# Optimization experiments

Hardware: AMD Instinct MI355X
Metric: run time of the kernel (lower is better)

The kernel has to match this reference:

```python
import jax, jax.numpy as jnp
import numpy as np

N_EDGE_TYPES = 25
EF = 2  # edge feature dim (excluding type)
HID = 10


def _edge_nn(et, ef, emb, wh, bh, wg, bg):
    # y = relu(emb[et] * (ef@Wh+bh) + (ef@Wg+bg)) -> [E, in*out]
    return jax.nn.relu(emb[et] * (ef @ wh + bh) + (ef @ wg + bg))


def _nnconv(x, et, ef, src, dst, emb, wh, bh, wg, bg, root, bias, in_c, out_c):
    n = x.shape[0]
    w = _edge_nn(et, ef, emb, wh, bh, wg, bg).reshape(-1, in_c, out_c)  # [E,in,out]
    msg = jnp.einsum('ei,eio->eo', x[src], w)                          # per-edge matmul
    s = jax.ops.segment_sum(msg, dst, num_segments=n)
    cnt = jax.ops.segment_sum(jnp.ones((src.shape[0],), x.dtype), dst, num_segments=n)
    agg = s / jnp.maximum(cnt, 1.0)[:, None]                           # scatter-mean
    return agg + x @ root + bias


def _make_params(key, in_c, out_c):
    ks = jax.random.split(key, 6)
    d = in_c * out_c
    s = 0.1
    return dict(
        emb=jax.random.normal(ks[0], (N_EDGE_TYPES, d), jnp.float32) * s,
        wh=jax.random.normal(ks[1], (EF, d), jnp.float32) * s,
        bh=jax.random.normal(ks[2], (d,), jnp.float32) * s,
        wg=jax.random.normal(ks[3], (EF, d), jnp.float32) * s,
        bg=jax.random.normal(ks[4], (d,), jnp.float32) * s,
        root=jax.random.normal(ks[5], (in_c, out_c), jnp.float32) * s,
        bias=jnp.zeros((out_c,), jnp.float32),
    )


def setup_inputs() -> dict:
    key = jax.random.key(0)
    ks = jax.random.split(key, 12)
    N, E, IN_C, OUT_C, B = 50000, 250000, 16, 16, 8
    inp = {
        'x': jax.random.normal(ks[0], (N, IN_C), jnp.float32),
        'edge_feat': jax.random.normal(ks[1], (E, EF), jnp.float32),
        'edge_type': jax.random.randint(ks[2], (E,), 0, N_EDGE_TYPES),
        'edge_src': jax.random.randint(ks[3], (E,), 0, N),
        'edge_dst': jax.random.randint(ks[4], (E,), 0, N),
        'cell_type': jax.random.randint(ks[5], (N,), 0, 3),
        'batch_ids': jnp.sort(jax.random.randint(ks[6], (N,), 0, B)),
        'batch_size': B,
    }
    for i, (ic, oc) in enumerate([(IN_C, HID), (HID, HID), (HID, OUT_C)], start=1):
        p = _make_params(ks[6 + i], ic, oc)
        for k, v in p.items():
            inp[f'{k}{i}'] = v
    return inp


def reference(x, edge_feat,
              emb1, wh1, bh1, wg1, bg1, root1, bias1,
              emb2, wh2, bh2, wg2, bg2, root2, bias2,
              emb3, wh3, bh3, wg3, bg3, root3, bias3,
              edge_type, edge_src, edge_dst, cell_type, batch_ids, batch_size):
    in_c, out_c = x.shape[1], root3.shape[1]
    h = _nnconv(x, edge_type, edge_feat, edge_src, edge_dst,
                emb1, wh1, bh1, wg1, bg1, root1, bias1, in_c, HID)
    h = jax.nn.relu(h)  # dropout is identity in eval mode
    h = _nnconv(h, edge_type, edge_feat, edge_src, edge_dst,
                emb2, wh2, bh2, wg2, bg2, root2, bias2, HID, HID)
    h = jax.nn.relu(h)
    h = _nnconv(h, edge_type, edge_feat, edge_src, edge_dst,
                emb3, wh3, bh3, wg3, bg3, root3, bias3, HID, out_c)
    h = jax.nn.relu(h)
    # scatter-mean pooling over nodes with cell_type==1, grouped by graph id
    gate = (cell_type == 1).astype(jnp.int32)
    idx = gate * (batch_ids.astype(jnp.int32) + 1)  # 0 = discarded bucket
    nseg = batch_size + 1
    s = jax.ops.segment_sum(h, idx, num_segments=nseg)
    cnt = jax.ops.segment_sum(jnp.ones((h.shape[0],), h.dtype), idx, num_segments=nseg)
    pooled = s / jnp.maximum(cnt, 1.0)[:, None]
    return pooled[1:batch_size + 1, :]  # [B, out_c]
```

## Files before the change

### kernel.cpp

```cpp
#include <hip/hip_runtime.h>

#define IN1 16
#define HIDC 10
#define OUT3 16
#define NTYPES 25
#define MAXB 32
#define HSTR 12

__global__ __launch_bounds__(256) void zero2_kernel(int* __restrict__ a, int na,
                                                    int* __restrict__ b, int nb) {
  int i = blockIdx.x * blockDim.x + threadIdx.x;
  int s = gridDim.x * blockDim.x;
  for (int j = i; j < na; j += s) a[j] = 0;
  for (int j = i; j < nb; j += s) b[j] = 0;
}

__global__ __launch_bounds__(256) void hist_kernel(const int* __restrict__ edst,
                                                   int* __restrict__ deg,
                                                   int* __restrict__ pos, int E) {
  int e = blockIdx.x * blockDim.x + threadIdx.x;
  if (e < E) pos[e] = atomicAdd(&deg[edst[e]], 1);
}

__global__ __launch_bounds__(1024) void scan_kernel(const int4* __restrict__ deg4,
                                                    int* __restrict__ row_ptr, int N) {
  __shared__ int wsums[16];
  __shared__ int s_run;
  int tid = threadIdx.x, lane = tid & 63, wid = tid >> 6;
  if (tid == 0) s_run = 0;
  __syncthreads();
  int N4 = (N + 3) >> 2;
  for (int base = 0; base < N4; base += 1024) {
    int i4 = base + tid;
    int4 v = make_int4(0, 0, 0, 0);
    if (i4 < N4) v = deg4[i4];
    int idx0 = i4 * 4;
    if (idx0 + 1 >= N) v.y = 0;
    if (idx0 + 2 >= N) v.z = 0;
    if (idx0 + 3 >= N) v.w = 0;
    int s = v.x + v.y + v.z + v.w;
    int x = s;
    #pragma unroll
    for (int off = 1; off < 64; off <<= 1) {
      int y = __shfl_up(x, off);
      if (lane >= off) x += y;
    }
    if (lane == 63) wsums[wid] = x;
    __syncthreads();
    if (tid < 16) {
      int w = wsums[tid];
      #pragma unroll
      for (int off = 1; off < 16; off <<= 1) {
        int y = __shfl_up(w, off);
        if (tid >= off) w += y;
      }
      wsums[tid] = w;
    }
    __syncthreads();
    int excl = x - s + ((wid > 0) ? wsums[wid - 1] : 0) + s_run;
    int total = wsums[15];
    if (idx0 < N) row_ptr[idx0] = excl;
    if (idx0 + 1 < N) row_ptr[idx0 + 1] = excl + v.x;
    if (idx0 + 2 < N) row_ptr[idx0 + 2] = excl + v.x + v.y;
    if (idx0 + 3 < N) row_ptr[idx0 + 3] = excl + v.x + v.y + v.z;
    __syncthreads();
    if (tid == 0) s_run += total;
    __syncthreads();
  }
  if (threadIdx.x == 0) row_ptr[N] = s_run;
}

__global__ __launch_bounds__(256) void permute_kernel(
    const int* __restrict__ edst, const int* __restrict__ esrc,
    const int* __restrict__ et, const float2* __restrict__ ef,
    const int* __restrict__ row_ptr, const int* __restrict__ pos,
    int4* __restrict__ edges, int E) {
  int e = blockIdx.x * blockDim.x + threadIdx.x;
  if (e >= E) return;
  int d = edst[e];
  int idx = row_ptr[d] + pos[e];
  float2 f = ef[e];
  int4 r;
  r.x = esrc[e];
  r.y = et[e];
  r.z = __float_as_int(f.x);
  r.w = __float_as_int(f.y);
  edges[idx] = r;
}

template<int IN_C, int XSTR, int O>
__device__ void pack_one(int t, const float* emb, const float* wh, const float* bh,
                         const float* wg, const float* bg,
                         float4* gAB, float2* gC) {
  constexpr int D = IN_C * O;
  constexpr int NI2 = XSTR / 2;
  for (int idx = threadIdx.x; idx < NI2 * O; idx += 256) {
    int i2 = idx / O, o = idx - i2 * O;
    int i0 = 2 * i2, i1 = 2 * i2 + 1;
    float a0 = 0.f, b0 = 0.f, c0 = 0.f, a1 = 0.f, b1 = 0.f, c1 = 0.f;
    if (i0 < IN_C) {
      int k = i0 * O + o;
      float e = emb[t * D + k];
      a0 = fmaf(e, wh[k], wg[k]);
      b0 = fmaf(e, wh[D + k], wg[D + k]);
      c0 = fmaf(e, bh[k], bg[k]);
    }
    if (i1 < IN_C) {
      int k = i1 * O + o;
      float e = emb[t * D + k];
      a1 = fmaf(e, wh[k], wg[k]);
      b1 = fmaf(e, wh[D + k], wg[D + k]);
      c1 = fmaf(e, bh[k], bg[k]);
    }
    int kk = (i2 * NTYPES + t) * O + o;
    gAB[kk] = make_float4(a0, b0, a1, b1);
    gC[kk] = make_float2(c0, c1);
  }
}

__global__ __launch_bounds__(256) void abc_pack_kernel(
    const float* __restrict__ emb1, const float* __restrict__ wh1,
    const float* __restrict__ bh1, const float* __restrict__ wg1, const float* __restrict__ bg1,
    const float* __restrict__ emb2, const float* __restrict__ wh2,
    const float* __restrict__ bh2, const float* __restrict__ wg2, const float* __restrict__ bg2,
    const float* __restrict__ emb3, const float* __restrict__ wh3,
    const float* __restrict__ bh3, const float* __restrict__ wg3, const float* __restrict__ bg3,
    float4* __restrict__ gAB1, float2* __restrict__ gC1,
    float4* __restrict__ gAB2, float2* __restrict__ gC2,
    float4* __restrict__ gAB3, float2* __restrict__ gC3)
{
  int t = blockIdx.x;
  pack_one<IN1, 16, HIDC>(t, emb1, wh1, bh1, wg1, bg1, gAB1, gC1);
  pack_one<HIDC, HSTR, HIDC>(t, emb2, wh2, bh2, wg2, bg2, gAB2, gC2);
  pack_one<HIDC, HSTR, OUT3>(t, emb3, wh3, bh3, wg3, bg3, gAB3, gC3);
}

template<int IN_C, int XSTR, int O, int IPG, int NPW, bool POOL>
__global__ __launch_bounds__(512, 6) void layer_kernel(
    const float* __restrict__ xin,
    const int4* __restrict__ edges,
    const int* __restrict__ row_ptr,
    const float4* __restrict__ gAB,
    const float2* __restrict__ gC,
    const float* __restrict__ root,
    const float* __restrict__ bias,
    float* __restrict__ hout,
    const int* __restrict__ ctype, const int* __restrict__ bids,
    float* __restrict__ pcnt, int N, int B)
{
  constexpr int NI2 = XSTR / 2;
  constexpr int SZ = NI2 * NTYPES * O;
  constexpr int IC = XSTR / IPG;
  constexpr int NPB = 8 * NPW;
  __shared__ __align__(16) float4 s_AB[SZ];
  __shared__ __align__(16) float2 s_C[SZ];
  __shared__ float s_root[IN_C * O];
  __shared__ float s_bias[O];
  __shared__ float s_psum[POOL ? (MAXB * 16) : 1];
  __shared__ float s_pcnt[POOL ? MAXB : 1];

  int tid = threadIdx.x;
  for (int k = tid; k < SZ; k += 512) s_AB[k] = gAB[k];
  {
    const float4* gc4 = (const float4*)gC;
    float4* sc4 = (float4*)s_C;
    for (int k = tid; k < SZ / 2; k += 512) sc4[k] = gc4[k];
  }
  for (int k = tid; k < IN_C * O; k += 512) s_root[k] = root[k];
  if (tid < O) s_bias[tid] = bias[tid];
  if (POOL) {
    for (int i = tid; i < MAXB * 16; i += 512) s_psum[i] = 0.f;
    for (int i = tid; i < MAXB; i += 512) s_pcnt[i] = 0.f;
  }
  __syncthreads();

  int wave = tid >> 6, lane = tid & 63;
  int slot = lane / (16 * IPG);
  int rem = lane % (16 * IPG);
  int ig = rem >> 4;
  int o = rem & 15;
  int oc = (o < O) ? o : (O - 1);

  int n = blockIdx.x * NPB + wave * NPW + slot;
  int start = 0, end = 0;
  if (n < N) { start = row_ptr[n]; end = row_ptr[n + 1]; }
  float acc = 0.f;
  int4 r = (start < end) ? edges[start] : make_int4(0, 0, 0, 0);
  for (int e = start; e < end;) {
    int4 cur = r;
    ++e;
    if (e < end) r = edges[e];
    int src = cur.x, t = cur.y;
    float f0 = __int_as_float(cur.z), f1 = __int_as_float(cur.w);
    const float* __restrict__ xr = xin + (size_t)src * XSTR + ig * IC;
    float xv[IC];
    if (IC == 4) {
      float4 v = *(const float4*)xr;
      xv[0] = v.x; xv[1] = v.y; xv[2] = v.z; xv[3] = v.w;
    } else {
      const float2* x2 = (const float2*)xr;
      float2 a = x2[0], b = x2[1], c = x2[2];
      xv[0] = a.x; xv[1] = a.y; xv[2] = b.x; xv[3] = b.y; xv[4] = c.x; xv[5] = c.y;
    }
    #pragma unroll
    for (int j = 0; j < IC / 2; ++j) {
      int i2 = ig * (IC / 2) + j;
      int k = (i2 * NTYPES + t) * O + oc;
      float4 ab = s_AB[k];
      float2 c2 = s_C[k];
      float w0 = fmaxf(fmaf(f0, ab.x, fmaf(f1, ab.y, c2.x)), 0.f);
      float w1 = fmaxf(fmaf(f0, ab.z, fmaf(f1, ab.w, c2.y)), 0.f);
      acc = fmaf(xv[2 * j], w0, acc);
      acc = fmaf(xv[2 * j + 1], w1, acc);
    }
  }
  acc += __shfl_xor(acc, 16);
  if (IPG == 4) acc += __shfl_xor(acc, 32);

  if (n < N && ig == 0 && o < O) {
    float inv = 1.0f / fmaxf((float)(end - start), 1.0f);
    float v = fmaf(acc, inv, s_bias[o]);
    const float* __restrict__ xr = xin + (size_t)n * XSTR;
    #pragma unroll
    for (int i = 0; i < IN_C; ++i) v = fmaf(xr[i], s_root[i * O + o], v);
    v = fmaxf(v, 0.f);
    if (!POOL) {
      hout[(size_t)n * HSTR + o] = v;
    } else if (ctype[n] == 1) {
      int b = bids[n];
      atomicAdd(&s_psum[b * 16 + o], v);
      if (o == 0) atomicAdd(&s_pcnt[b], 1.0f);
    }
  }

  if (POOL) {
    __syncthreads();
    for (int i = tid; i < B * 16; i += 512) {
      float v = s_psum[i];
      if (v != 0.f) atomicAdd(&hout[i], v);
    }
    for (int i = tid; i < B; i += 512) {
      float c = s_pcnt[i];
      if (c != 0.f) atomicAdd(&pcnt[i], c);
    }
  }
}

__global__ __launch_bounds__(256) void finalize_kernel(
    const float* __restrict__ psum, const float* __restrict__ pcnt,
    float* __restrict__ out, int B) {
  int i = blockIdx.x * blockDim.x + threadIdx.x;
  if (i >= B * OUT3) return;
  int b = i / OUT3;
  out[i] = psum[i] / fmaxf(pcnt[b], 1.0f);
}

extern "C" void kernel_launch(void* const* d_in, const int* in_sizes, int n_in,
                              void* d_out, int out_size, void* d_ws, size_t ws_size,
                              hipStream_t stream)
{
  const float* x     = (const float*)d_in[0];
  const float* ef    = (const float*)d_in[1];
  const int*   et    = (const int*)d_in[2];
  const int*   esrc  = (const int*)d_in[3];
  const int*   edst  = (const int*)d_in[4];
  const int*   ctype = (const int*)d_in[5];
  const int*   bids  = (const int*)d_in[6];
  const float* emb1 = (const float*)d_in[8];
  const float* wh1  = (const float*)d_in[9];
  const float* bh1  = (const float*)d_in[10];
  const float* wg1  = (const float*)d_in[11];
  const float* bg1  = (const float*)d_in[12];
  const float* root1= (const float*)d_in[13];
  const float* bias1= (const float*)d_in[14];
  const float* emb2 = (const float*)d_in[15];
  const float* wh2  = (const float*)d_in[16];
  const float* bh2  = (const float*)d_in[17];
  const float* wg2  = (const float*)d_in[18];
  const float* bg2  = (const float*)d_in[19];
  const float* root2= (const float*)d_in[20];
  const float* bias2= (const float*)d_in[21];
  const float* emb3 = (const float*)d_in[22];
  const float* wh3  = (const float*)d_in[23];
  const float* bh3  = (const float*)d_in[24];
  const float* wg3  = (const float*)d_in[25];
  const float* bg3  = (const float*)d_in[26];
  const float* root3= (const float*)d_in[27];
  const float* bias3= (const float*)d_in[28];

  const int N = in_sizes[0] / IN1;
  const int E = in_sizes[2];
  const int B = out_size / OUT3;

  int4* edges   = (int4*)d_ws;
  int*  deg     = (int*)(edges + E);
  int*  pos     = deg + N;
  int*  row_ptr = pos + E;
  int   np1r    = ((N + 1 + 3) / 4) * 4;
  float* h1     = (float*)(row_ptr + np1r);
  float* h2     = h1 + (size_t)N * HSTR;
  float* psum   = h2 + (size_t)N * HSTR;
  float* pcnt   = psum + (size_t)B * 16;
  float* pk     = pcnt + B;
  float4* gAB1 = (float4*)pk;
  float2* gC1  = (float2*)(pk + 8000);
  float4* gAB2 = (float4*)(pk + 12000);
  float2* gC2  = (float2*)(pk + 18000);
  float4* gAB3 = (float4*)(pk + 21000);
  float2* gC3  = (float2*)(pk + 30600);

  zero2_kernel<<<128, 256, 0, stream>>>(deg, N, (int*)psum, B * 16 + B);
  abc_pack_kernel<<<NTYPES, 256, 0, stream>>>(
      emb1, wh1, bh1, wg1, bg1, emb2, wh2, bh2, wg2, bg2, emb3, wh3, bh3, wg3, bg3,
      gAB1, gC1, gAB2, gC2, gAB3, gC3);
  hist_kernel<<<(E + 255) / 256, 256, 0, stream>>>(edst, deg, pos, E);
  scan_kernel<<<1, 1024, 0, stream>>>((const int4*)deg, row_ptr, N);
  permute_kernel<<<(E + 255) / 256, 256, 0, stream>>>(
      edst, esrc, et, (const float2*)ef, row_ptr, pos, edges, E);

  layer_kernel<IN1, 16, HIDC, 4, 1, false><<<(N + 7) / 8, 512, 0, stream>>>(
      x, edges, row_ptr, gAB1, gC1, root1, bias1, h1, nullptr, nullptr, nullptr, N, B);
  layer_kernel<HIDC, HSTR, HIDC, 2, 2, false><<<(N + 15) / 16, 512, 0, stream>>>(
      h1, edges, row_ptr, gAB2, gC2, root2, bias2, h2, nullptr, nullptr, nullptr, N, B);
  layer_kernel<HIDC, HSTR, OUT3, 2, 2, true><<<(N + 15) / 16, 512, 0, stream>>>(
      h2, edges, row_ptr, gAB3, gC3, root3, bias3, psum, ctype, bids, pcnt, N, B);

  finalize_kernel<<<1, 256, 0, stream>>>(psum, pcnt, (float*)d_out, B);
}
```

Baseline: 301.4 us.

## Fuse zeroing into pack kernel, trim padded pairs, unroll edge loop by two

Merges the zeroing kernel into the parameter-pack kernel, saving one launch. The packed tables now cover only the real input channels instead of the padded stride, which shrinks shared memory and removes wasted FMAs for layers 2 and 3. The edge loop is unrolled by two with independent accumulators to raise memory-level parallelism, replacing the explicit one-ahead prefetch. The IPG=2 split becomes uneven (3 pairs versus 2), which adds lane imbalance and a predicated branch.

```diff
diff --git a/kernel.cpp b/kernel.cpp
--- a/kernel.cpp
+++ b/kernel.cpp
@@ -6,14 +6,6 @@
 #define NTYPES 25
 #define MAXB 32
 #define HSTR 12
-
-__global__ __launch_bounds__(256) void zero2_kernel(int* __restrict__ a, int na,
-                                                    int* __restrict__ b, int nb) {
-  int i = blockIdx.x * blockDim.x + threadIdx.x;
-  int s = gridDim.x * blockDim.x;
-  for (int j = i; j < na; j += s) a[j] = 0;
-  for (int j = i; j < nb; j += s) b[j] = 0;
-}
 
 __global__ __launch_bounds__(256) void hist_kernel(const int* __restrict__ edst,
                                                    int* __restrict__ deg,
@@ -88,37 +80,29 @@
   edges[idx] = r;
 }
 
-template<int IN_C, int XSTR, int O>
+template<int IN_C, int O>
 __device__ void pack_one(int t, const float* emb, const float* wh, const float* bh,
                          const float* wg, const float* bg,
                          float4* gAB, float2* gC) {
   constexpr int D = IN_C * O;
-  constexpr int NI2 = XSTR / 2;
+  constexpr int NI2 = IN_C / 2;
   for (int idx = threadIdx.x; idx < NI2 * O; idx += 256) {
     int i2 = idx / O, o = idx - i2 * O;
-    int i0 = 2 * i2, i1 = 2 * i2 + 1;
-    float a0 = 0.f, b0 = 0.f, c0 = 0.f, a1 = 0.f, b1 = 0.f, c1 = 0.f;
-    if (i0 < IN_C) {
-      int k = i0 * O + o;
-      float e = emb[t * D + k];
-      a0 = fmaf(e, wh[k], wg[k]);
-      b0 = fmaf(e, wh[D + k], wg[D + k]);
-      c0 = fmaf(e, bh[k], bg[k]);
-    }
-    if (i1 < IN_C) {
-      int k = i1 * O + o;
-      float e = emb[t * D + k];
-      a1 = fmaf(e, wh[k], wg[k]);
-      b1 = fmaf(e, wh[D + k], wg[D + k]);
-      c1 = fmaf(e, bh[k], bg[k]);
-    }
+    int k0 = (2 * i2) * O + o, k1 = k0 + O;
+    float e0 = emb[t * D + k0], e1 = emb[t * D + k1];
+    float a0 = fmaf(e0, wh[k0], wg[k0]);
+    float b0 = fmaf(e0, wh[D + k0], wg[D + k0]);
+    float c0 = fmaf(e0, bh[k0], bg[k0]);
+    float a1 = fmaf(e1, wh[k1], wg[k1]);
+    float b1 = fmaf(e1, wh[D + k1], wg[D + k1]);
+    float c1 = fmaf(e1, bh[k1], bg[k1]);
     int kk = (i2 * NTYPES + t) * O + o;
     gAB[kk] = make_float4(a0, b0, a1, b1);
     gC[kk] = make_float2(c0, c1);
   }
 }
 
-__global__ __launch_bounds__(256) void abc_pack_kernel(
+__global__ __launch_bounds__(256) void pack_zero_kernel(
     const float* __restrict__ emb1, const float* __restrict__ wh1,
     const float* __restrict__ bh1, const float* __restrict__ wg1, const float* __restrict__ bg1,
     const float* __restrict__ emb2, const float* __restrict__ wh2,
@@ -127,12 +111,20 @@
     const float* __restrict__ bh3, const float* __restrict__ wg3, const float* __restrict__ bg3,
     float4* __restrict__ gAB1, float2* __restrict__ gC1,
     float4* __restrict__ gAB2, float2* __restrict__ gC2,
-    float4* __restrict__ gAB3, float2* __restrict__ gC3)
+    float4* __restrict__ gAB3, float2* __restrict__ gC3,
+    int* __restrict__ za, int na, int* __restrict__ zb, int nb)
 {
-  int t = blockIdx.x;
-  pack_one<IN1, 16, HIDC>(t, emb1, wh1, bh1, wg1, bg1, gAB1, gC1);
-  pack_one<HIDC, HSTR, HIDC>(t, emb2, wh2, bh2, wg2, bg2, gAB2, gC2);
-  pack_one<HIDC, HSTR, OUT3>(t, emb3, wh3, bh3, wg3, bg3, gAB3, gC3);
+  if (blockIdx.x < NTYPES) {
+    int t = blockIdx.x;
+    pack_one<IN1, HIDC>(t, emb1, wh1, bh1, wg1, bg1, gAB1, gC1);
+    pack_one<HIDC, HIDC>(t, emb2, wh2, bh2, wg2, bg2, gAB2, gC2);
+    pack_one<HIDC, OUT3>(t, emb3, wh3, bh3, wg3, bg3, gAB3, gC3);
+  } else {
+    int bi = blockIdx.x - NTYPES;
+    int nthr = (gridDim.x - NTYPES) * 256;
+    for (int i = bi * 256 + threadIdx.x; i < na; i += nthr) za[i] = 0;
+    for (int i = bi * 256 + threadIdx.x; i < nb; i += nthr) zb[i] = 0;
+  }
 }
 
 template<int IN_C, int XSTR, int O, int IPG, int NPW, bool POOL>
@@ -148,9 +140,9 @@
     const int* __restrict__ ctype, const int* __restrict__ bids,
     float* __restrict__ pcnt, int N, int B)
 {
-  constexpr int NI2 = XSTR / 2;
+  constexpr int NI2 = IN_C / 2;
   constexpr int SZ = NI2 * NTYPES * O;
-  constexpr int IC = XSTR / IPG;
+  constexpr int JMAX = (IPG == 4) ? 2 : 3;
   constexpr int NPB = 8 * NPW;
   __shared__ __align__(16) float4 s_AB[SZ];
   __shared__ __align__(16) float2 s_C[SZ];
@@ -181,39 +173,54 @@
   int o = rem & 15;
   int oc = (o < O) ? o : (O - 1);
 
+  int npair, i2b, ch0;
+  if (IPG == 4) { npair = 2; i2b = ig * 2; ch0 = ig * 4; }
+  else { npair = (ig == 0) ? 3 : 2; i2b = (ig == 0) ? 0 : 3; ch0 = (ig == 0) ? 0 : 6; }
+
   int n = blockIdx.x * NPB + wave * NPW + slot;
   int start = 0, end = 0;
   if (n < N) { start = row_ptr[n]; end = row_ptr[n + 1]; }
-  float acc = 0.f;
-  int4 r = (start < end) ? edges[start] : make_int4(0, 0, 0, 0);
-  for (int e = start; e < end;) {
-    int4 cur = r;
-    ++e;
-    if (e < end) r = edges[e];
+
+  auto body = [&](int4 cur, float& a) {
     int src = cur.x, t = cur.y;
     float f0 = __int_as_float(cur.z), f1 = __int_as_float(cur.w);
-    const float* __restrict__ xr = xin + (size_t)src * XSTR + ig * IC;
-    float xv[IC];
-    if (IC == 4) {
+    const float* __restrict__ xr = xin + (size_t)src * XSTR + ch0;
+    float xv[2 * JMAX];
+    if (IPG == 4) {
       float4 v = *(const float4*)xr;
       xv[0] = v.x; xv[1] = v.y; xv[2] = v.z; xv[3] = v.w;
     } else {
       const float2* x2 = (const float2*)xr;
-      float2 a = x2[0], b = x2[1], c = x2[2];
-      xv[0] = a.x; xv[1] = a.y; xv[2] = b.x; xv[3] = b.y; xv[4] = c.x; xv[5] = c.y;
-    }
+      float2 p0 = x2[0], p1 = x2[1], p2 = x2[2];
+      xv[0] = p0.x; xv[1] = p0.y; xv[2] = p1.x; xv[3] = p1.y; xv[4] = p2.x; xv[5] = p2.y;
+    }
+    int kb = t * O + oc;
     #pragma unroll
-    for (int j = 0; j < IC / 2; ++j) {
-      int i2 = ig * (IC / 2) + j;
-      int k = (i2 * NTYPES + t) * O + oc;
-      float4 ab = s_AB[k];
-      float2 c2 = s_C[k];
-      float w0 = fmaxf(fmaf(f0, ab.x, fmaf(f1, ab.y, c2.x)), 0.f);
-      float w1 = fmaxf(fmaf(f0, ab.z, fmaf(f1, ab.w, c2.y)), 0.f);
-      acc = fmaf(xv[2 * j], w0, acc);
-      acc = fmaf(xv[2 * j + 1], w1, acc);
-    }
-  }
+    for (int j = 0; j < JMAX; ++j) {
+      bool on = (IPG == 4) || (j < npair);
+      if (on) {
+        int k = (i2b + j) * (NTYPES * O) + kb;
+        float4 ab = s_AB[k];
+        float2 c2 = s_C[k];
+        float w0 = fmaxf(fmaf(f0, ab.x, fmaf(f1, ab.y, c2.x)), 0.f);
+        float w1 = fmaxf(fmaf(f0, ab.z, fmaf(f1, ab.w, c2.y)), 0.f);
+        a = fmaf(xv[2 * j], w0, a);
+        a = fmaf(xv[2 * j + 1], w1, a);
+      }
+    }
+  };
+
+  float acc0 = 0.f, acc1 = 0.f;
+  int e = start;
+  for (; e + 1 < end; e += 2) {
+    int4 c0 = edges[e];
+    int4 c1 = edges[e + 1];
+    body(c0, acc0);
+    body(c1, acc1);
+  }
+  if (e < end) body(edges[e], acc0);
+  float acc = acc0 + acc1;
+
   acc += __shfl_xor(acc, 16);
   if (IPG == 4) acc += __shfl_xor(acc, 32);
 
@@ -305,14 +312,14 @@
   float4* gAB1 = (float4*)pk;
   float2* gC1  = (float2*)(pk + 8000);
   float4* gAB2 = (float4*)(pk + 12000);
-  float2* gC2  = (float2*)(pk + 18000);
-  float4* gAB3 = (float4*)(pk + 21000);
-  float2* gC3  = (float2*)(pk + 30600);
-
-  zero2_kernel<<<128, 256, 0, stream>>>(deg, N, (int*)psum, B * 16 + B);
-  abc_pack_kernel<<<NTYPES, 256, 0, stream>>>(
+  float2* gC2  = (float2*)(pk + 17000);
+  float4* gAB3 = (float4*)(pk + 19504);
+  float2* gC3  = (float2*)(pk + 27504);
+
+  pack_zero_kernel<<<160, 256, 0, stream>>>(
       emb1, wh1, bh1, wg1, bg1, emb2, wh2, bh2, wg2, bg2, emb3, wh3, bh3, wg3, bg3,
-      gAB1, gC1, gAB2, gC2, gAB3, gC3);
+      gAB1, gC1, gAB2, gC2, gAB3, gC3,
+      deg, N, (int*)psum, B * 16 + B);
   hist_kernel<<<(E + 255) / 256, 256, 0, stream>>>(edst, deg, pos, E);
   scan_kernel<<<1, 1024, 0, stream>>>((const int4*)deg, row_ptr, N);
   permute_kernel<<<(E + 255) / 256, 256, 0, stream>>>(
```

After: 302.4 us. About the same (+0.4%).
